# Performance work log

Hardware: AMD Instinct MI355X
Metric: run time of the kernel (lower is better)

Reference implementation:

```python
import jax, jax.numpy as jnp
import numpy as np

B, N, L, D, H = 8, 128, 4096, 1024, 16

def setup_inputs() -> dict:
    key = jax.random.key(0)
    ks = jax.random.split(key, 7)
    s = 1.0 / np.sqrt(D)  # xavier-ish scale for square D x D weights
    return {
        "q": jax.random.normal(ks[0], (B, N, D), dtype=jnp.float32),
        "k": jax.random.normal(ks[1], (B, L, D), dtype=jnp.float32),
        "v": jax.random.normal(ks[2], (B, L, D), dtype=jnp.float32),
        "Wq": jax.random.normal(ks[3], (D, D), dtype=jnp.float32) * s,
        "Wk": jax.random.normal(ks[4], (D, D), dtype=jnp.float32) * s,
        "Wv": jax.random.normal(ks[5], (D, D), dtype=jnp.float32) * s,
        "Wo": jax.random.normal(ks[6], (D, D), dtype=jnp.float32) * s,
    }

def reference(q, k, v, Wq, Wk, Wv, Wo):
    Bq, Nq, Dm = q.shape
    Lk = k.shape[1]
    Hh = H
    Dh = Dm // Hh
    scale = Dm ** (-0.5)  # note: scaled by d_model, not head_dim (faithful to source)
    # projections (nn.Linear with weight (out,in): y = x @ W.T)
    qh = (q @ Wq.T).reshape(Bq, Nq, Hh, Dh).transpose(0, 2, 1, 3)  # B H N Dh
    kh = (k @ Wk.T).reshape(Bq, Lk, Hh, Dh).transpose(0, 2, 1, 3)  # B H L Dh
    vh = (v @ Wv.T).reshape(Bq, Lk, Hh, Dh).transpose(0, 2, 1, 3)  # B H L Dh
    attn = jnp.einsum('bhnc,bhlc->bhnl', qh * scale, kh)          # B H N L
    # inverted attention: softmax over the query (N) axis...
    attn = jax.nn.softmax(attn, axis=2)
    # ...then L1-renormalize over the key (L) axis
    attn = attn / jnp.sum(attn, axis=-1, keepdims=True)
    out = jnp.einsum('bhnl,bhlc->bhnc', attn, vh)                 # B H N Dh
    out = out.transpose(0, 2, 1, 3).reshape(Bq, Nq, Dm)
    return out @ Wo.T
```

## Files before the change

### kernel.cpp

```cpp
#include <hip/hip_runtime.h>
#include <stdint.h>

typedef __bf16 bf16_t;
typedef __bf16 bf16x4 __attribute__((ext_vector_type(4)));
typedef __bf16 bf16x8 __attribute__((ext_vector_type(8)));
typedef float f32x4 __attribute__((ext_vector_type(4)));
typedef unsigned int u32;

constexpr int CB = 8, CN = 128, CL = 4096, CD = 1024, CH = 16, CDh = 64;

#define BAR()                                    \
  do {                                           \
    __asm__ volatile("" ::: "memory");           \
    __builtin_amdgcn_s_barrier();                \
    __asm__ volatile("" ::: "memory");           \
  } while (0)

__device__ __forceinline__ bf16x4 cvt4(float4 v) {
  bf16x4 r;
  r[0] = (__bf16)v.x; r[1] = (__bf16)v.y; r[2] = (__bf16)v.z; r[3] = (__bf16)v.w;
  return r;
}

__device__ __forceinline__ void async16(void* lds, const void* g) {
  __builtin_amdgcn_global_load_lds(
      (const __attribute__((address_space(1))) u32*)g,
      (__attribute__((address_space(3))) u32*)lds, 16, 0, 0);
}

__global__ __launch_bounds__(256) void cvt_f32_bf16(const float* __restrict__ in,
                                                    bf16_t* __restrict__ outp, int n4) {
  int i = (int)blockIdx.x * 256 + (int)threadIdx.x;
  if (i < n4) {
    float4 v = reinterpret_cast<const float4*>(in)[i];
    reinterpret_cast<bf16x4*>(outp)[i] = cvt4(v);
  }
}

__global__ __launch_bounds__(256)
void cvt3(const float* __restrict__ q, const float* __restrict__ k,
          const float* __restrict__ v, bf16_t* __restrict__ qc,
          bf16_t* __restrict__ kc, bf16_t* __restrict__ vc,
          int n4q, int n4kv) {
  int i = (int)blockIdx.x * 256 + (int)threadIdx.x;
  const float* src;
  bf16_t* dst;
  int idx;
  if (i < n4q) { src = q; dst = qc; idx = i; }
  else if (i < n4q + n4kv) { src = k; dst = kc; idx = i - n4q; }
  else if (i < n4q + 2 * n4kv) { src = v; dst = vc; idx = i - n4q - n4kv; }
  else return;
  reinterpret_cast<bf16x4*>(dst)[idx] = cvt4(reinterpret_cast<const float4*>(src)[idx]);
}

__global__ __launch_bounds__(256)
void cvt_w4(const float* __restrict__ Wq, const float* __restrict__ Wk,
            const float* __restrict__ Wv, const float* __restrict__ Wo,
            bf16_t* __restrict__ outp, int n4) {
  const float* srcs[4] = {Wq, Wk, Wv, Wo};
  const float* s = srcs[blockIdx.y];
  int i = (int)blockIdx.x * 256 + (int)threadIdx.x;
  if (i < n4)
    reinterpret_cast<bf16x4*>(outp + (size_t)blockIdx.y * CD * CD)[i] =
        cvt4(reinterpret_cast<const float4*>(s)[i]);
}

__global__ __launch_bounds__(512, 2)
void gemm8(const bf16_t* __restrict__ A0, const bf16_t* __restrict__ Bw0,
           bf16_t* __restrict__ C0, const bf16_t* __restrict__ A1,
           const bf16_t* __restrict__ Bw1, bf16_t* __restrict__ C1,
           int N, int K) {
  __shared__ __attribute__((aligned(16))) char lds[131072];

  const int t = (int)threadIdx.x;
  const int lane = t & 63, w = t >> 6;
  const int wave_m = w >> 2, wave_n = w & 3;
  const int fr = lane & 15, fq = lane >> 4;
  const int bid = (int)blockIdx.x;
  const int x = bid & 7, j = bid >> 3;
  const bool second = (A1 != nullptr) && (j >= 64);
  const int jj = second ? (j - 64) : j;
  const bf16_t* A  = second ? A1 : A0;
  const bf16_t* Bw = second ? Bw1 : Bw0;
  bf16_t* C        = second ? C1 : C0;
  const int mb = x * 16 + (jj >> 2);
  const int nb = jj & 3;
  const int brow = mb * 256, bcol = nb * 256;

  auto Aoff = [](int buf, int half) { return (buf * 2 + half) * 16384; };
  auto Boff = [](int buf, int half) { return 65536 + (buf * 2 + half) * 16384; };

  auto stage = [&](int tile, bool dA, bool dB) {
    const int buf = tile & 1;
    const int k0 = tile << 6;
#pragma unroll
    for (int n = 0; n < 2; ++n) {
      const int idx = n * 512 + t;
      const int row = idx >> 3;
      const int u = (idx & 7) ^ (row & 7);
      const int dst = (n * 8 + w) * 1024;
      if (dB) {
#pragma unroll
        for (int h = 0; h < 2; ++h)
          async16(lds + Boff(buf, h) + dst,
                  Bw + (size_t)(bcol + h * 128 + row) * K + k0 + u * 8);
      }
      if (dA) {
#pragma unroll
        for (int h = 0; h < 2; ++h)
          async16(lds + Aoff(buf, h) + dst,
                  A + (size_t)(brow + h * 128 + row) * K + k0 + u * 8);
      }
    }
  };

  bf16x8 af[4][2], blo[2][2], bhi[2][2];
  auto rdA = [&](int buf, int mq) {
    const char* base = lds + Aoff(buf, wave_m);
#pragma unroll
    for (int mf = 0; mf < 4; ++mf) {
      const int row = mq * 64 + mf * 16 + fr;
#pragma unroll
      for (int ks = 0; ks < 2; ++ks)
        af[mf][ks] = *(const bf16x8*)(base + row * 128 + (((ks * 4 + fq) ^ (row & 7)) << 4));
    }
  };
  auto rdB = [&](bf16x8 (&bf)[2][2], int buf, int nq) {
    const char* base = lds + Boff(buf, wave_n >> 1);
#pragma unroll
    for (int nf = 0; nf < 2; ++nf) {
      const int row = (wave_n & 1) * 64 + (nq * 2 + nf) * 16 + fr;
#pragma unroll
      for (int ks = 0; ks < 2; ++ks)
        bf[nf][ks] = *(const bf16x8*)(base + row * 128 + (((ks * 4 + fq) ^ (row & 7)) << 4));
    }
  };

  const f32x4 z = {0.f, 0.f, 0.f, 0.f};
  f32x4 acc[8][4];
#pragma unroll
  for (int m = 0; m < 8; ++m)
#pragma unroll
    for (int n = 0; n < 4; ++n) acc[m][n] = z;

  auto mma = [&](const bf16x8 (&bf)[2][2], int mq, int nq) {
    __builtin_amdgcn_s_setprio(1);
#pragma unroll
    for (int mf = 0; mf < 4; ++mf)
#pragma unroll
      for (int nf = 0; nf < 2; ++nf)
#pragma unroll
        for (int ks = 0; ks < 2; ++ks)
          acc[mq * 4 + mf][nq * 2 + nf] = __builtin_amdgcn_mfma_f32_16x16x32_bf16(
              af[mf][ks], bf[nf][ks], acc[mq * 4 + mf][nq * 2 + nf], 0, 0, 0);
    __builtin_amdgcn_s_setprio(0);
  };

  const int nt = K >> 6;
  stage(0, true, true);
  stage(1, true, true);
  asm volatile("s_waitcnt vmcnt(8)" ::: "memory");
  BAR();

  for (int i = 0; i < nt; ++i) {
    const int buf = i & 1;
    rdA(buf, 0);
    rdB(blo, buf, 0);
    BAR();
    mma(blo, 0, 0);
    BAR();
    rdB(bhi, buf, 1);
    BAR();
    mma(bhi, 0, 1);
    BAR();
    rdA(buf, 1);
    if (i + 2 < nt) stage(i + 2, false, true);
    BAR();
    mma(blo, 1, 0);
    BAR();
    if (i + 2 < nt) stage(i + 2, true, false);
    if (i == nt - 2) {
      asm volatile("s_waitcnt vmcnt(0)" ::: "memory");
    } else if (i < nt - 2) {
      asm volatile("s_waitcnt vmcnt(8)" ::: "memory");
    }
    BAR();
    mma(bhi, 1, 1);
    BAR();
  }

#pragma unroll
  for (int mf = 0; mf < 8; ++mf)
#pragma unroll
    for (int nf = 0; nf < 4; ++nf)
#pragma unroll
      for (int r = 0; r < 4; ++r) {
        const int row = brow + wave_m * 128 + mf * 16 + fq * 4 + r;
        const int col = bcol + wave_n * 64 + nf * 16 + fr;
        C[(size_t)row * N + col] = (__bf16)acc[mf][nf][r];
      }
}

template<bool CF32>
__global__ __launch_bounds__(256)
void gemm_dma(const bf16_t* __restrict__ Ab, const bf16_t* __restrict__ Bw,
              void* __restrict__ Cp, int mblocks, int N, int K) {
  __shared__ __attribute__((aligned(16))) char AsB[2][8192];
  __shared__ __attribute__((aligned(16))) char BsB[2][8192];

  const int t = (int)threadIdx.x;
  const int lane = t & 63, wv = t >> 6;
  const int bid = (int)blockIdx.x;
  const int x = bid & 7;
  const int j = bid >> 3;
  const int S = mblocks >> 3;
  const int mb = (S > 0) ? (x * S + (j >> 3)) : (j >> 3);
  const int nb = j & 7;
  const int brow = mb * 128;
  const int bcol = nb * 128;
  const int wm = (wv >> 1) * 64, wn = (wv & 1) * 64;
  const int fr = lane & 15, fq = lane >> 4;

  auto stageT = [&](char* dst, const bf16_t* src, int rbase, int k0) {
    const int r4 = lane >> 2, u = lane & 3;
#pragma unroll
    for (int i = 0; i < 2; ++i) {
      const int seg = i * 4 + wv;
      const int row = seg * 16 + r4;
      const int col = ((u ^ ((row >> 1) & 3)) << 3);
      async16(dst + seg * 1024, src + (size_t)(rbase + row) * K + k0 + col);
    }
  };

  const f32x4 z = {0.f, 0.f, 0.f, 0.f};
  f32x4 acc[4][4];
#pragma unroll
  for (int m = 0; m < 4; ++m)
#pragma unroll
    for (int n = 0; n < 4; ++n) acc[m][n] = z;

  const int nt = K >> 5;
  stageT(AsB[0], Ab, brow, 0);
  stageT(BsB[0], Bw, bcol, 0);
  __syncthreads();
  int cur = 0;

  for (int tt = 0; tt < nt; ++tt) {
    if (tt + 1 < nt) {
      stageT(AsB[cur ^ 1], Ab, brow, (tt + 1) << 5);
      stageT(BsB[cur ^ 1], Bw, bcol, (tt + 1) << 5);
    }
    const char* Ac = AsB[cur];
    const char* Bc = BsB[cur];

    bf16x8 af[4], bfg[4];
#pragma unroll
    for (int m = 0; m < 4; ++m) {
      const int R = wm + m * 16 + fr;
      const int ph = (fq << 4) ^ (((R >> 1) & 3) << 4);
      af[m] = *(const bf16x8*)(Ac + R * 64 + ph);
    }
#pragma unroll
    for (int n = 0; n < 4; ++n) {
      const int R = wn + n * 16 + fr;
      const int ph = (fq << 4) ^ (((R >> 1) & 3) << 4);
      bfg[n] = *(const bf16x8*)(Bc + R * 64 + ph);
    }
#pragma unroll
    for (int m = 0; m < 4; ++m)
#pragma unroll
      for (int n = 0; n < 4; ++n)
        acc[m][n] = __builtin_amdgcn_mfma_f32_16x16x32_bf16(af[m], bfg[n], acc[m][n], 0, 0, 0);

    __syncthreads();
    cur ^= 1;
  }

  const int rb = fq * 4;
#pragma unroll
  for (int m = 0; m < 4; ++m)
#pragma unroll
    for (int n = 0; n < 4; ++n)
#pragma unroll
      for (int r = 0; r < 4; ++r) {
        const int row = brow + wm + m * 16 + rb + r;
        const int col = bcol + wn + n * 16 + fr;
        if constexpr (CF32)
          ((float*)Cp)[(size_t)row * N + col] = acc[m][n][r];
        else
          ((bf16_t*)Cp)[(size_t)row * N + col] = (__bf16)acc[m][n][r];
      }
}

template<bool A_IS_F32, bool C_IS_F32>
__global__ __launch_bounds__(256)
void gemm_bt(const void* __restrict__ Ap, const float* __restrict__ Bw,
             void* __restrict__ Cp, int M, int N, int K) {
  (void)M;
  __shared__ bf16_t As[128][40];
  __shared__ bf16_t Bs[128][40];
  const int t = (int)threadIdx.x;
  const int lane = t & 63, wv = t >> 6;
  const int wm = (wv >> 1) * 64, wn = (wv & 1) * 64;
  const int brow = (int)blockIdx.y * 128, bcol = (int)blockIdx.x * 128;
  const int fr = lane & 15, fk = (lane >> 4) * 8;

  const f32x4 z = {0.f, 0.f, 0.f, 0.f};
  f32x4 acc[4][4];
#pragma unroll
  for (int m = 0; m < 4; ++m)
#pragma unroll
    for (int n = 0; n < 4; ++n) acc[m][n] = z;

  for (int k0 = 0; k0 < K; k0 += 32) {
    if constexpr (A_IS_F32) {
      const float* A = (const float*)Ap;
      const int tr = t >> 3, tc = (t & 7) * 4;
#pragma unroll
      for (int p = 0; p < 4; ++p) {
        const int r = p * 32 + tr;
        float4 v = *reinterpret_cast<const float4*>(A + (size_t)(brow + r) * K + k0 + tc);
        *reinterpret_cast<bf16x4*>(&As[r][tc]) = cvt4(v);
      }
    } else {
      const bf16_t* A = (const bf16_t*)Ap;
      const int tr = t >> 2, tc = (t & 3) * 8;
#pragma unroll
      for (int p = 0; p < 2; ++p) {
        const int r = p * 64 + tr;
        *reinterpret_cast<int4*>(&As[r][tc]) =
            *reinterpret_cast<const int4*>(A + (size_t)(brow + r) * K + k0 + tc);
      }
    }
    {
      const int tr = t >> 3, tc = (t & 7) * 4;
#pragma unroll
      for (int p = 0; p < 4; ++p) {
        const int r = p * 32 + tr;
        float4 v = *reinterpret_cast<const float4*>(Bw + (size_t)(bcol + r) * K + k0 + tc);
        *reinterpret_cast<bf16x4*>(&Bs[r][tc]) = cvt4(v);
      }
    }
    __syncthreads();
    bf16x8 af[4], bfr[4];
#pragma unroll
    for (int m = 0; m < 4; ++m)
      af[m] = *reinterpret_cast<const bf16x8*>(&As[wm + m * 16 + fr][fk]);
#pragma unroll
    for (int n = 0; n < 4; ++n)
      bfr[n] = *reinterpret_cast<const bf16x8*>(&Bs[wn + n * 16 + fr][fk]);
#pragma unroll
    for (int m = 0; m < 4; ++m)
#pragma unroll
      for (int n = 0; n < 4; ++n)
        acc[m][n] = __builtin_amdgcn_mfma_f32_16x16x32_bf16(af[m], bfr[n], acc[m][n], 0, 0, 0);
    __syncthreads();
  }
  const int rb = (lane >> 4) * 4;
#pragma unroll
  for (int m = 0; m < 4; ++m)
#pragma unroll
    for (int n = 0; n < 4; ++n)
#pragma unroll
      for (int r = 0; r < 4; ++r) {
        const int row = brow + wm + m * 16 + rb + r;
        const int col = bcol + wn + n * 16 + fr;
        if constexpr (C_IS_F32)
          ((float*)Cp)[(size_t)row * N + col] = acc[m][n][r];
        else
          ((bf16_t*)Cp)[(size_t)row * N + col] = (__bf16)acc[m][n][r];
      }
}

template<bool DIRECT>
__global__ __launch_bounds__(256)
void attn_inv(const bf16_t* __restrict__ qh, const bf16_t* __restrict__ kh,
              const bf16_t* __restrict__ vh, bf16_t* __restrict__ ao,
              float* __restrict__ part, int lcount) {
  const int bh = (int)blockIdx.x;
  const int b = bh >> 4, h = bh & 15;
  const int l_begin = (int)blockIdx.y * lcount;

  __shared__ bf16_t Qs[128][72];
  __shared__ bf16_t Ks[64][72];
  __shared__ bf16_t Vt[80][72];
  __shared__ bf16_t Ps[128][72];

  const int t = (int)threadIdx.x;
  const int lane = t & 63, w = t >> 6;
  const int fr = lane & 15, fq = lane >> 4;

  const bf16_t* qb = qh + (size_t)(b * CN) * CD + h * CDh;
#pragma unroll
  for (int p = 0; p < 4; ++p) {
    const int j = p * 256 + t;
    const int r = j >> 3, cc = (j & 7) * 8;
    *reinterpret_cast<int4*>(&Qs[r][cc]) =
        *reinterpret_cast<const int4*>(qb + (size_t)r * CD + cc);
  }
#pragma unroll
  for (int p = 0; p < 4; ++p) {
    const int j = p * 256 + t;
    const int r = 64 + (j >> 6), c = j & 63;
    Vt[r][c] = (r == 64) ? (__bf16)1.0f : (__bf16)0.0f;
  }

  const f32x4 z = {0.f, 0.f, 0.f, 0.f};
  f32x4 acc[2][5];
#pragma unroll
  for (int m = 0; m < 2; ++m)
#pragma unroll
    for (int n = 0; n < 5; ++n) acc[m][n] = z;

  for (int l0 = l_begin; l0 < l_begin + lcount; l0 += 64) {
    __syncthreads();
    const bf16_t* kb = kh + (size_t)(b * CL + l0) * CD + h * CDh;
    const bf16_t* vb = vh + (size_t)(b * CL + l0) * CD + h * CDh;
#pragma unroll
    for (int p = 0; p < 2; ++p) {
      const int j = p * 256 + t;
      const int r = j >> 3, cc = (j & 7) * 8;
      *reinterpret_cast<int4*>(&Ks[r][cc]) =
          *reinterpret_cast<const int4*>(kb + (size_t)r * CD + cc);
      int4 vv = *reinterpret_cast<const int4*>(vb + (size_t)r * CD + cc);
      const bf16_t* hp = reinterpret_cast<const bf16_t*>(&vv);
#pragma unroll
      for (int i = 0; i < 8; ++i) Vt[cc + i][r] = hp[i];
    }
    __syncthreads();

    f32x4 s[8];
#pragma unroll
    for (int m = 0; m < 8; ++m) s[m] = z;
#pragma unroll
    for (int ks = 0; ks < 2; ++ks) {
      bf16x8 bk = *reinterpret_cast<const bf16x8*>(&Ks[w * 16 + fr][ks * 32 + fq * 8]);
#pragma unroll
      for (int m = 0; m < 8; ++m) {
        bf16x8 aq = *reinterpret_cast<const bf16x8*>(&Qs[m * 16 + fr][ks * 32 + fq * 8]);
        s[m] = __builtin_amdgcn_mfma_f32_16x16x32_bf16(aq, bk, s[m], 0, 0, 0);
      }
    }

    float p[8][4];
    float mx = -3.0e38f;
#pragma unroll
    for (int m = 0; m < 8; ++m)
#pragma unroll
      for (int r = 0; r < 4; ++r) {
        const float xv = s[m][r] * 0.03125f;
        p[m][r] = xv;
        mx = fmaxf(mx, xv);
      }
    mx = fmaxf(mx, __shfl_xor(mx, 16));
    mx = fmaxf(mx, __shfl_xor(mx, 32));
    float sum = 0.f;
#pragma unroll
    for (int m = 0; m < 8; ++m)
#pragma unroll
      for (int r = 0; r < 4; ++r) {
        const float e = __expf(p[m][r] - mx);
        p[m][r] = e;
        sum += e;
      }
    sum += __shfl_xor(sum, 16);
    sum += __shfl_xor(sum, 32);
    const float inv = 1.0f / sum;
    const int pcol = w * 16 + fr;
#pragma unroll
    for (int m = 0; m < 8; ++m)
#pragma unroll
      for (int r = 0; r < 4; ++r)
        Ps[m * 16 + fq * 4 + r][pcol] = (__bf16)(p[m][r] * inv);
    __syncthreads();

#pragma unroll
    for (int ks = 0; ks < 2; ++ks) {
      bf16x8 pa[2];
#pragma unroll
      for (int m = 0; m < 2; ++m)
        pa[m] = *reinterpret_cast<const bf16x8*>(&Ps[w * 32 + m * 16 + fr][ks * 32 + fq * 8]);
#pragma unroll
      for (int n = 0; n < 5; ++n) {
        bf16x8 bv = *reinterpret_cast<const bf16x8*>(&Vt[n * 16 + fr][ks * 32 + fq * 8]);
#pragma unroll
        for (int m = 0; m < 2; ++m)
          acc[m][n] = __builtin_amdgcn_mfma_f32_16x16x32_bf16(pa[m], bv, acc[m][n], 0, 0, 0);
      }
    }
  }

  if constexpr (DIRECT) {
    bf16_t* ob = ao + (size_t)(b * CN) * CD + h * CDh;
#pragma unroll
    for (int m = 0; m < 2; ++m)
#pragma unroll
      for (int r = 0; r < 4; ++r) {
        const float R = __shfl(acc[m][4][r], lane & 48);
        const float invr = 1.0f / R;
        const int row = w * 32 + m * 16 + fq * 4 + r;
#pragma unroll
        for (int n = 0; n < 4; ++n) {
          const int col = n * 16 + fr;
          ob[(size_t)row * CD + col] = (__bf16)(acc[m][n][r] * invr);
        }
      }
  } else {
    float* pb = part + ((size_t)blockIdx.y * (CB * CH) + bh) * (size_t)(CN * 72);
#pragma unroll
    for (int m = 0; m < 2; ++m)
#pragma unroll
      for (int r = 0; r < 4; ++r) {
        const int row = w * 32 + m * 16 + fq * 4 + r;
#pragma unroll
        for (int n = 0; n < 4; ++n)
          pb[(size_t)row * 72 + n * 16 + fr] = acc[m][n][r];
        if (fr == 0) pb[(size_t)row * 72 + 64] = acc[m][4][r];
      }
  }
}

__global__ __launch_bounds__(256)
void attn_reduce(const float* __restrict__ part, bf16_t* __restrict__ ao, int nsplit) {
  const int idx = (int)blockIdx.x * 256 + (int)threadIdx.x;
  const int c = idx & 63;
  const int n = (idx >> 6) & 127;
  const int bh = idx >> 13;
  const float* p = part + (size_t)bh * (CN * 72) + (size_t)n * 72;
  const size_t sstr = (size_t)(CB * CH) * (CN * 72);
  float o = 0.f, r = 0.f;
  for (int s = 0; s < nsplit; ++s) {
    o += p[(size_t)s * sstr + c];
    r += p[(size_t)s * sstr + 64];
  }
  const int b = bh >> 4, h = bh & 15;
  ao[((size_t)(b * CN + n)) * CD + h * CDh + c] = (__bf16)(o / r);
}

extern "C" void kernel_launch(void* const* d_in, const int* in_sizes, int n_in,
                              void* d_out, int out_size, void* d_ws, size_t ws_size,
                              hipStream_t stream) {
  (void)in_sizes; (void)n_in; (void)out_size;
  const float* q  = (const float*)d_in[0];
  const float* k  = (const float*)d_in[1];
  const float* v  = (const float*)d_in[2];
  const float* Wq = (const float*)d_in[3];
  const float* Wk = (const float*)d_in[4];
  const float* Wv = (const float*)d_in[5];
  const float* Wo = (const float*)d_in[6];
  float* out = (float*)d_out;

  const size_t MiB = (size_t)1 << 20;
  const size_t QH_OFF = 0;
  const size_t KH_OFF = 2 * MiB;
  const size_t VH_OFF = KH_OFF + 64 * MiB;
  const size_t AO_OFF = VH_OFF + 64 * MiB;
  const size_t FIXED  = AO_OFF + 2 * MiB;
  if (ws_size < FIXED) return;

  char* ws = (char*)d_ws;
  bf16_t* qh = (bf16_t*)(ws + QH_OFF);
  bf16_t* kh = (bf16_t*)(ws + KH_OFF);
  bf16_t* vh = (bf16_t*)(ws + VH_OFF);
  bf16_t* ao = (bf16_t*)(ws + AO_OFF);

  const int M_q = CB * CN;
  const int M_kv = CB * CL;
  const int W4 = CD * CD / 4;
  const int A4_kv = M_kv * CD / 4;
  const int A4_q  = M_q * CD / 4;
  const size_t WS = (size_t)CD * CD;
  const size_t PB = (size_t)CB * CH * CN * 72 * 4;

  const size_t WB4_OFF = FIXED;
  const size_t QC_OFF  = WB4_OFF + 8 * MiB;
  const size_t KC_OFF  = QC_OFF + 2 * MiB;
  const size_t VC_OFF  = KC_OFF + 64 * MiB;
  const size_t NEED_A  = VC_OFF + 64 * MiB;

  if (ws_size >= NEED_A) {
    bf16_t* wb4 = (bf16_t*)(ws + WB4_OFF);
    bf16_t* qc  = (bf16_t*)(ws + QC_OFF);
    bf16_t* kc  = (bf16_t*)(ws + KC_OFF);
    bf16_t* vc  = (bf16_t*)(ws + VC_OFF);
    float* part = (float*)(ws + KC_OFF);

    cvt_w4<<<dim3(W4 / 256, 4), 256, 0, stream>>>(Wq, Wk, Wv, Wo, wb4, W4);
    const int n4tot = A4_q + 2 * A4_kv;
    cvt3<<<(n4tot + 255) / 256, 256, 0, stream>>>(q, k, v, qc, kc, vc, A4_q, A4_kv);

    gemm_dma<false><<<(M_q / 128) * 8, 256, 0, stream>>>(qc, wb4, qh, M_q / 128, CD, CD);
    gemm8<<<1024, 512, 0, stream>>>(kc, wb4 + WS, kh, vc, wb4 + 2 * WS, vh, CD, CD);

    attn_inv<false><<<dim3(CB * CH, 8), 256, 0, stream>>>(qh, kh, vh, ao, part, CL / 8);
    attn_reduce<<<(CB * CH * CN * 64) / 256, 256, 0, stream>>>(part, ao, 8);

    gemm_dma<true><<<(M_q / 128) * 8, 256, 0, stream>>>(ao, wb4 + 3 * WS, out, M_q / 128, CD, CD);
    return;
  }

  const size_t WBUF_OFF = FIXED;
  const size_t QCB_OFF  = WBUF_OFF + 2 * MiB;
  const size_t KCB_OFF  = QCB_OFF + 2 * MiB;
  const size_t NEED_B   = KCB_OFF + 64 * MiB;

  if (ws_size >= NEED_B) {
    bf16_t* wbuf = (bf16_t*)(ws + WBUF_OFF);
    bf16_t* qc   = (bf16_t*)(ws + QCB_OFF);
    bf16_t* kc   = (bf16_t*)(ws + KCB_OFF);
    float*  part = (float*)(ws + KCB_OFF);

    cvt_f32_bf16<<<A4_q / 256, 256, 0, stream>>>(q, qc, A4_q);
    cvt_f32_bf16<<<W4 / 256, 256, 0, stream>>>(Wq, wbuf, W4);
    gemm_dma<false><<<(M_q / 128) * 8, 256, 0, stream>>>(qc, wbuf, qh, M_q / 128, CD, CD);

    cvt_f32_bf16<<<A4_kv / 256, 256, 0, stream>>>(k, kc, A4_kv);
    cvt_f32_bf16<<<W4 / 256, 256, 0, stream>>>(Wk, wbuf, W4);
    gemm8<<<512, 512, 0, stream>>>(kc, wbuf, kh, nullptr, nullptr, nullptr, CD, CD);

    cvt_f32_bf16<<<A4_kv / 256, 256, 0, stream>>>(v, kc, A4_kv);
    cvt_f32_bf16<<<W4 / 256, 256, 0, stream>>>(Wv, wbuf, W4);
    gemm8<<<512, 512, 0, stream>>>(kc, wbuf, vh, nullptr, nullptr, nullptr, CD, CD);

    attn_inv<false><<<dim3(CB * CH, 8), 256, 0, stream>>>(qh, kh, vh, ao, part, CL / 8);
    attn_reduce<<<(CB * CH * CN * 64) / 256, 256, 0, stream>>>(part, ao, 8);

    cvt_f32_bf16<<<W4 / 256, 256, 0, stream>>>(Wo, wbuf, W4);
    gemm_dma<true><<<(M_q / 128) * 8, 256, 0, stream>>>(ao, wbuf, out, M_q / 128, CD, CD);
    return;
  }

  gemm_bt<true, false><<<dim3(CD / 128, M_q / 128),  256, 0, stream>>>(q, Wq, qh, M_q,  CD, CD);
  gemm_bt<true, false><<<dim3(CD / 128, M_kv / 128), 256, 0, stream>>>(k, Wk, kh, M_kv, CD, CD);
  gemm_bt<true, false><<<dim3(CD / 128, M_kv / 128), 256, 0, stream>>>(v, Wv, vh, M_kv, CD, CD);
  attn_inv<true><<<dim3(CB * CH, 1), 256, 0, stream>>>(qh, kh, vh, ao, nullptr, CL);
  gemm_bt<false, true><<<dim3(CD / 128, M_q / 128), 256, 0, stream>>>(ao, Wo, out, M_q, CD, CD);
}
```

Baseline: 335.9 us.

## Fuse input/weight conversion and Q projection into one kernel launch

Replaces the separate weight-conversion, q/k/v conversion and Q-projection GEMM launches with one kernel. The first 64 blocks compute the Q projection directly from fp32 q and Wq, converting to bf16 while staging into LDS, and the remaining blocks convert the weights and K/V. This removes two launches, the qc intermediate buffer and its round trip through memory. The trade-off is that the Q GEMM now uses a simple synchronous LDS tile loop instead of the DMA-pipelined GEMM.

```diff
diff --git a/kernel.cpp b/kernel.cpp
--- a/kernel.cpp
+++ b/kernel.cpp
@@ -38,31 +38,89 @@
 }
 
 __global__ __launch_bounds__(256)
-void cvt3(const float* __restrict__ q, const float* __restrict__ k,
-          const float* __restrict__ v, bf16_t* __restrict__ qc,
-          bf16_t* __restrict__ kc, bf16_t* __restrict__ vc,
-          int n4q, int n4kv) {
-  int i = (int)blockIdx.x * 256 + (int)threadIdx.x;
-  const float* src;
-  bf16_t* dst;
-  int idx;
-  if (i < n4q) { src = q; dst = qc; idx = i; }
-  else if (i < n4q + n4kv) { src = k; dst = kc; idx = i - n4q; }
-  else if (i < n4q + 2 * n4kv) { src = v; dst = vc; idx = i - n4q - n4kv; }
-  else return;
-  reinterpret_cast<bf16x4*>(dst)[idx] = cvt4(reinterpret_cast<const float4*>(src)[idx]);
-}
-
-__global__ __launch_bounds__(256)
-void cvt_w4(const float* __restrict__ Wq, const float* __restrict__ Wk,
-            const float* __restrict__ Wv, const float* __restrict__ Wo,
-            bf16_t* __restrict__ outp, int n4) {
-  const float* srcs[4] = {Wq, Wk, Wv, Wo};
-  const float* s = srcs[blockIdx.y];
-  int i = (int)blockIdx.x * 256 + (int)threadIdx.x;
-  if (i < n4)
-    reinterpret_cast<bf16x4*>(outp + (size_t)blockIdx.y * CD * CD)[i] =
-        cvt4(reinterpret_cast<const float4*>(s)[i]);
+void fuse1(const float* __restrict__ q, const float* __restrict__ k,
+           const float* __restrict__ v, const float* __restrict__ Wq,
+           const float* __restrict__ Wk, const float* __restrict__ Wv,
+           const float* __restrict__ Wo, bf16_t* __restrict__ qh,
+           bf16_t* __restrict__ wb4, bf16_t* __restrict__ kc,
+           bf16_t* __restrict__ vc) {
+  const int bid = (int)blockIdx.x;
+  const int t = (int)threadIdx.x;
+
+  if (bid >= 64) {
+    const int W4 = CD * CD / 4;
+    const int A4_kv = CB * CL * CD / 4;
+    if (bid < 64 + 4096) {
+      const int widx = bid - 64;
+      const int which = widx >> 10;
+      const float* srcs[4] = {Wq, Wk, Wv, Wo};
+      const int i = (widx & 1023) * 256 + t;
+      reinterpret_cast<bf16x4*>(wb4 + (size_t)which * CD * CD)[i] =
+          cvt4(reinterpret_cast<const float4*>(srcs[which])[i]);
+    } else {
+      const int i = (bid - 64 - 4096) * 256 + t;
+      if (i < A4_kv)
+        reinterpret_cast<bf16x4*>(kc)[i] = cvt4(reinterpret_cast<const float4*>(k)[i]);
+      else
+        reinterpret_cast<bf16x4*>(vc)[i - A4_kv] =
+            cvt4(reinterpret_cast<const float4*>(v)[i - A4_kv]);
+    }
+    return;
+  }
+
+  __shared__ bf16_t As[128][40];
+  __shared__ bf16_t Bs[128][40];
+  const int lane = t & 63, wv = t >> 6;
+  const int wm = (wv >> 1) * 64, wn = (wv & 1) * 64;
+  const int brow = (bid >> 3) * 128, bcol = (bid & 7) * 128;
+  const int fr = lane & 15, fk = (lane >> 4) * 8;
+  const int K = CD;
+
+  const f32x4 z = {0.f, 0.f, 0.f, 0.f};
+  f32x4 acc[4][4];
+#pragma unroll
+  for (int m = 0; m < 4; ++m)
+#pragma unroll
+    for (int n = 0; n < 4; ++n) acc[m][n] = z;
+
+  for (int k0 = 0; k0 < K; k0 += 32) {
+    {
+      const int tr = t >> 3, tc = (t & 7) * 4;
+#pragma unroll
+      for (int p = 0; p < 4; ++p) {
+        const int r = p * 32 + tr;
+        float4 va = *reinterpret_cast<const float4*>(q + (size_t)(brow + r) * K + k0 + tc);
+        *reinterpret_cast<bf16x4*>(&As[r][tc]) = cvt4(va);
+        float4 vb = *reinterpret_cast<const float4*>(Wq + (size_t)(bcol + r) * K + k0 + tc);
+        *reinterpret_cast<bf16x4*>(&Bs[r][tc]) = cvt4(vb);
+      }
+    }
+    __syncthreads();
+    bf16x8 af[4], bfr[4];
+#pragma unroll
+    for (int m = 0; m < 4; ++m)
+      af[m] = *reinterpret_cast<const bf16x8*>(&As[wm + m * 16 + fr][fk]);
+#pragma unroll
+    for (int n = 0; n < 4; ++n)
+      bfr[n] = *reinterpret_cast<const bf16x8*>(&Bs[wn + n * 16 + fr][fk]);
+#pragma unroll
+    for (int m = 0; m < 4; ++m)
+#pragma unroll
+      for (int n = 0; n < 4; ++n)
+        acc[m][n] = __builtin_amdgcn_mfma_f32_16x16x32_bf16(af[m], bfr[n], acc[m][n], 0, 0, 0);
+    __syncthreads();
+  }
+  const int rb = (lane >> 4) * 4;
+#pragma unroll
+  for (int m = 0; m < 4; ++m)
+#pragma unroll
+    for (int n = 0; n < 4; ++n)
+#pragma unroll
+      for (int r = 0; r < 4; ++r) {
+        const int row = brow + wm + m * 16 + rb + r;
+        const int col = bcol + wn + n * 16 + fr;
+        qh[(size_t)row * CD + col] = (__bf16)acc[m][n][r];
+      }
 }
 
 __global__ __launch_bounds__(512, 2)
@@ -580,16 +638,15 @@
 
   if (ws_size >= NEED_A) {
     bf16_t* wb4 = (bf16_t*)(ws + WB4_OFF);
-    bf16_t* qc  = (bf16_t*)(ws + QC_OFF);
     bf16_t* kc  = (bf16_t*)(ws + KC_OFF);
     bf16_t* vc  = (bf16_t*)(ws + VC_OFF);
     float* part = (float*)(ws + KC_OFF);
 
-    cvt_w4<<<dim3(W4 / 256, 4), 256, 0, stream>>>(Wq, Wk, Wv, Wo, wb4, W4);
-    const int n4tot = A4_q + 2 * A4_kv;
-    cvt3<<<(n4tot + 255) / 256, 256, 0, stream>>>(q, k, v, qc, kc, vc, A4_q, A4_kv);
-
-    gemm_dma<false><<<(M_q / 128) * 8, 256, 0, stream>>>(qc, wb4, qh, M_q / 128, CD, CD);
+    const int NB_W = 4096;
+    const int NB_KV = 2 * A4_kv / 256;
+    fuse1<<<64 + NB_W + NB_KV, 256, 0, stream>>>(q, k, v, Wq, Wk, Wv, Wo,
+                                                 qh, wb4, kc, vc);
+
     gemm8<<<1024, 512, 0, stream>>>(kc, wb4 + WS, kh, vc, wb4 + 2 * WS, vh, CD, CD);
 
     attn_inv<false><<<dim3(CB * CH, 8), 256, 0, stream>>>(qh, kh, vh, ao, part, CL / 8);
```

New measurement: 333.8 us, median of 2. No clear change (-0.6%).
